# Optimization experiments

Measured on AMD Instinct MI355X. Metric: run time of the kernel, lower is better.

Reference implementation:

```python
import jax, jax.numpy as jnp
import numpy as np

B, S, L, Q = 128, 200, 50, 20   # batch, story sentences, sentence len, query len
V, D, K = 50000, 128, 3          # vocab, embed dim, n_hops


def _pe(J, d):
    # position encoding l_kj = (1 - j/J) - (k/d)(1 - 2j/J), 1-indexed
    j = jnp.arange(1, J + 1, dtype=jnp.float32)[:, None]
    k = jnp.arange(1, d + 1, dtype=jnp.float32)[None, :]
    return 1.0 - j / J - (k / d) * (1.0 - 2.0 * j / J)  # (J, d)


def setup_inputs() -> dict:
    key = jax.random.key(0)
    ks = jax.random.split(key, 5)
    story = jax.random.randint(ks[0], (B, S, L), 0, V)
    query = jax.random.randint(ks[1], (B, Q), 0, V)
    # K+1 embedding tables (adjacent weight sharing: A^{k+1} = C^k), sigma=0.1, padding row 0 zeroed
    embs = (jax.random.normal(ks[2], (K + 1, V, D)) * 0.1).at[:, 0, :].set(0.0)
    TA = jax.random.normal(ks[3], (K, S, D)) * 0.1
    TC = jax.random.normal(ks[4], (K, S, D)) * 0.1
    return {"story": story, "query": query, "embs": embs, "TA": TA, "TC": TC}


def reference(story, query, embs, TA, TC):
    d = embs.shape[-1]
    pe_s = _pe(story.shape[-1], d)   # (L, D)
    pe_q = _pe(query.shape[-1], d)   # (Q, D)
    n_hops = TA.shape[0]

    # query embedding with PE: (B, Q, D) * (Q, D) -> sum over Q -> (B, D)
    u = (jnp.take(embs[0], query, axis=0) * pe_q).sum(axis=1)

    for hop in range(n_hops):
        # gather + PE multiply + sum over words + temporal encoding: (B, S, D)
        m = (jnp.take(embs[hop], story, axis=0) * pe_s).sum(axis=2) + TA[hop]
        c = (jnp.take(embs[hop + 1], story, axis=0) * pe_s).sum(axis=2) + TC[hop]
        # attention over memory slots
        p = jax.nn.softmax(jnp.einsum('bsd,bd->bs', m, u), axis=-1)  # (B, S)
        o = jnp.einsum('bs,bsd->bd', p, c)                            # (B, D)
        u = u + o

    # final projection W = embeddings[n_hops].weight -> logits (B, V)
    return u @ embs[n_hops].T
```

## Files before the change

kernel.cpp:

```cpp
#include <hip/hip_runtime.h>

#define B 128
#define S 200
#define LW 50
#define Q 20
#define V 50000
#define D 128
#define NH 3
#define VD (V * D)
#define BSD (B * S * D)
#define BS (B * S)

typedef __bf16 bf16x8 __attribute__((ext_vector_type(8)));
typedef float f32x4 __attribute__((ext_vector_type(4)));
typedef unsigned int u32x4 __attribute__((ext_vector_type(4)));

__device__ __forceinline__ unsigned int f2bf_rne(float f) {
  union { float f; unsigned int u; } c; c.f = f;
  return (c.u + 0x7FFFu + ((c.u >> 16) & 1u)) >> 16;
}
__device__ __forceinline__ unsigned int pack2(float a, float b) {
  return f2bf_rne(a) | (f2bf_rne(b) << 16);
}
__device__ __forceinline__ float bf_lo(unsigned int q) {
  union { unsigned int u; float f; } c; c.u = q << 16; return c.f;
}
__device__ __forceinline__ float bf_hi(unsigned int q) {
  union { unsigned int u; float f; } c; c.u = q & 0xFFFF0000u; return c.f;
}

__global__ __launch_bounds__(256) void k_repack(
    const float* __restrict__ embs, unsigned int* __restrict__ ESM) {
  int v = blockIdx.x * 4 + (threadIdx.x >> 6);
  int l = threadIdx.x & 63;
  int s = l >> 4, c = l & 15;
#pragma unroll
  for (int k = 0; k < 4; ++k) {
    const float2 e = *(const float2*)(embs + (size_t)k * VD + (size_t)v * D + 2 * l);
    ESM[((size_t)(k * 4 + s) * V + v) * 16 + c] = pack2(e.x, e.y);
  }
}

__global__ __launch_bounds__(256) void k_story16(
    const int* __restrict__ story, unsigned short* __restrict__ story16) {
  int i = blockIdx.x * 256 + threadIdx.x;
  int4 v = ((const int4*)story)[i];
  ushort4 o;
  o.x = (unsigned short)v.x; o.y = (unsigned short)v.y;
  o.z = (unsigned short)v.z; o.w = (unsigned short)v.w;
  ((ushort4*)story16)[i] = o;
}

__global__ __launch_bounds__(256) void k_packT(
    const float* __restrict__ TA, const float* __restrict__ TC,
    unsigned int* __restrict__ TAp, unsigned int* __restrict__ TCp) {
  int idx = blockIdx.x * 256 + threadIdx.x;
  int row = idx >> 6;
  int u = idx & 63;
  int d0 = 32 * (u >> 4) + 2 * (u & 15);
  const float2 a = *(const float2*)(TA + (size_t)row * D + d0);
  const float2 c = *(const float2*)(TC + (size_t)row * D + d0);
  TAp[idx] = pack2(a.x, a.y);
  TCp[idx] = pack2(c.x, c.y);
}

__global__ __launch_bounds__(256) void k_gather_slice(
    const unsigned short* __restrict__ story16,
    const u32x4* __restrict__ ESM4, unsigned int* __restrict__ Gp, int phase) {
  __shared__ __align__(16) unsigned short sidx[4][800];
  int unit = blockIdx.x & 7;
  int k = 2 * phase + (unit >> 2);
  int s = unit & 3;
  int widx = blockIdx.x >> 3;
  int w = threadIdx.x >> 6;
  int l = threadIdx.x & 63;
  int g = l >> 2;
  int q = l & 3;
  const u32x4* src4 = ESM4 + (size_t)(k * 4 + s) * V * 4;
  int d0 = s * 32 + 8 * q;

  int sent16 = widx * 64 + w * 16;
  const u32x4* st4 = (const u32x4*)(story16 + sent16 * LW);
  u32x4* dst4 = (u32x4*)sidx[w];
#pragma unroll
  for (int m = 0; m < 2; ++m) {
    int e = l + m * 64;
    if (e < 100) dst4[e] = __builtin_nontemporal_load(st4 + e);
  }
  const unsigned int* wrow32 = (const unsigned int*)(sidx[w] + g * LW);
  float SA[8] = {0.f, 0.f, 0.f, 0.f, 0.f, 0.f, 0.f, 0.f};
  float SB[8] = {0.f, 0.f, 0.f, 0.f, 0.f, 0.f, 0.f, 0.f};
#pragma unroll
  for (int jb = 0; jb < 5; ++jb) {
    unsigned int ip[5];
#pragma unroll
    for (int i = 0; i < 5; ++i) ip[i] = wrow32[jb * 5 + i];
    u32x4 qv[10];
#pragma unroll
    for (int i = 0; i < 5; ++i) {
      qv[2 * i + 0] = src4[(size_t)(ip[i] & 0xFFFFu) * 4 + q];
      qv[2 * i + 1] = src4[(size_t)(ip[i] >> 16) * 4 + q];
    }
#pragma unroll
    for (int i = 0; i < 10; ++i) {
      int j = jb * 10 + i;
      float jj = (float)(j + 1) * (1.0f / LW);
      float al = 1.0f - jj;
      float bl = 2.0f * jj - 1.0f;
      u32x4 v = qv[i];
      float ee[8];
      ee[0] = bf_lo(v.x); ee[1] = bf_hi(v.x);
      ee[2] = bf_lo(v.y); ee[3] = bf_hi(v.y);
      ee[4] = bf_lo(v.z); ee[5] = bf_hi(v.z);
      ee[6] = bf_lo(v.w); ee[7] = bf_hi(v.w);
#pragma unroll
      for (int ii = 0; ii < 8; ++ii) {
        SA[ii] += ee[ii] * al;
        SB[ii] += ee[ii] * bl;
      }
    }
  }
  float kd[8];
#pragma unroll
  for (int i = 0; i < 8; ++i) kd[i] = (float)(d0 + i + 1) * (1.0f / D);
  int sent = sent16 + g;
  u32x4 og;
  og.x = pack2(SA[0] + kd[0] * SB[0], SA[1] + kd[1] * SB[1]);
  og.y = pack2(SA[2] + kd[2] * SB[2], SA[3] + kd[3] * SB[3]);
  og.z = pack2(SA[4] + kd[4] * SB[4], SA[5] + kd[5] * SB[5]);
  og.w = pack2(SA[6] + kd[6] * SB[6], SA[7] + kd[7] * SB[7]);
  __builtin_nontemporal_store(
      og, (u32x4*)(Gp + ((size_t)k * BS + sent) * 64 + s * 16) + q);
}

__global__ __launch_bounds__(1024) void k_hops(
    const unsigned int* __restrict__ G, const unsigned int* __restrict__ TAp,
    const unsigned int* __restrict__ TCp, const int* __restrict__ query,
    const float* __restrict__ emb0, unsigned int* __restrict__ ubf) {
  __shared__ float su[D];
  __shared__ float sp[S];
  __shared__ float sred[2];
  __shared__ float4 oacc[32][32];
  int b = blockIdx.x;
  int t = threadIdx.x;
  if (t < D) {
    float kd = (float)(t + 1) * (1.0f / D);
    float acc = 0.f;
    for (int q = 0; q < Q; ++q) {
      int idx = query[b * Q + q];
      float jj = (float)(q + 1) * (1.0f / Q);
      float pe = 1.0f - jj - kd * (1.0f - 2.0f * jj);
      acc += emb0[(size_t)idx * D + t] * pe;
    }
    su[t] = acc;
  }
  __syncthreads();
  for (int hop = 0; hop < NH; ++hop) {
    const unsigned int* Gm = G + ((size_t)hop * BS + (size_t)b * S) * 64;
    const unsigned int* Gc = G + ((size_t)(hop + 1) * BS + (size_t)b * S) * 64;
    const unsigned int* ta = TAp + (size_t)hop * S * 64;
    const unsigned int* tc = TCp + (size_t)hop * S * 64;
    if (t < 4 * S) {
      int sl = t >> 2, p = t & 3;
      const uint2* gr = (const uint2*)(Gm + (size_t)sl * 64 + p * 16);
      const uint2* tr = (const uint2*)(ta + (size_t)sl * 64 + p * 16);
      float sc = 0.f;
#pragma unroll
      for (int i = 0; i < 8; ++i) {
        uint2 g2 = gr[i];
        uint2 t2 = tr[i];
        int dd = p * 32 + 4 * i;
        sc += (bf_lo(g2.x) + bf_lo(t2.x)) * su[dd + 0];
        sc += (bf_hi(g2.x) + bf_hi(t2.x)) * su[dd + 1];
        sc += (bf_lo(g2.y) + bf_lo(t2.y)) * su[dd + 2];
        sc += (bf_hi(g2.y) + bf_hi(t2.y)) * su[dd + 3];
      }
      sc += __shfl_xor(sc, 1);
      sc += __shfl_xor(sc, 2);
      if (p == 0) sp[sl] = sc;
    }
    __syncthreads();
    if (t < 64) {
      float mx = -1e30f;
      for (int s = t; s < S; s += 64) mx = fmaxf(mx, sp[s]);
#pragma unroll
      for (int off = 1; off < 64; off <<= 1) mx = fmaxf(mx, __shfl_xor(mx, off));
      float sum = 0.f;
      for (int s = t; s < S; s += 64) sum += expf(sp[s] - mx);
#pragma unroll
      for (int off = 1; off < 64; off <<= 1) sum += __shfl_xor(sum, off);
      if (t == 0) { sred[0] = mx; sred[1] = sum; }
    }
    __syncthreads();
    float mx = sred[0];
    float inv = 1.0f / sred[1];
    if (t < S) sp[t] = expf(sp[t] - mx) * inv;
    __syncthreads();
    {
      int g = t >> 5, c = t & 31;
      float4 o4 = {0.f, 0.f, 0.f, 0.f};
      for (int s = g; s < S; s += 32) {
        float p = sp[s];
        uint2 g2 = *(const uint2*)(Gc + (size_t)s * 64 + 2 * c);
        uint2 t2 = *(const uint2*)(tc + (size_t)s * 64 + 2 * c);
        o4.x += p * (bf_lo(g2.x) + bf_lo(t2.x));
        o4.y += p * (bf_hi(g2.x) + bf_hi(t2.x));
        o4.z += p * (bf_lo(g2.y) + bf_lo(t2.y));
        o4.w += p * (bf_hi(g2.y) + bf_hi(t2.y));
      }
      oacc[g][c] = o4;
    }
    __syncthreads();
    if (t < 32) {
      int d0 = (t >> 3) * 32 + (t & 7) * 4;
      float4 o = oacc[0][t];
#pragma unroll
      for (int g = 1; g < 32; ++g) {
        float4 x = oacc[g][t];
        o.x += x.x; o.y += x.y; o.z += x.z; o.w += x.w;
      }
      su[d0 + 0] += o.x;
      su[d0 + 1] += o.y;
      su[d0 + 2] += o.z;
      su[d0 + 3] += o.w;
    }
    __syncthreads();
  }
  if (t < 64) ubf[b * 64 + t] = pack2(su[2 * t], su[2 * t + 1]);
}

__global__ __launch_bounds__(256) void k_logits_mfma(
    const uint4* __restrict__ ubf,
    const uint4* __restrict__ esm,
    float* __restrict__ out) {
  int wid = threadIdx.x >> 6;
  int l = threadIdx.x & 63;
  int lr = l & 15;
  int lk = l >> 4;
  int vbase = blockIdx.x * 128 + wid * 32;
  uint4 bfrag[2][4];
#pragma unroll
  for (int vs = 0; vs < 2; ++vs) {
    int v = vbase + vs * 16 + lr;
    if (v >= V) v = V - 1;
#pragma unroll
    for (int kk = 0; kk < 4; ++kk)
      bfrag[vs][kk] = esm[((size_t)(12 + kk) * V + v) * 4 + lk];
  }
  f32x4 acc[2][8];
#pragma unroll
  for (int vs = 0; vs < 2; ++vs)
#pragma unroll
    for (int m = 0; m < 8; ++m) {
      f32x4 z = {0.f, 0.f, 0.f, 0.f};
      acc[vs][m] = z;
    }
#pragma unroll
  for (int m = 0; m < 8; ++m) {
    uint4 afrag[4];
#pragma unroll
    for (int kk = 0; kk < 4; ++kk)
      afrag[kk] = ubf[(m * 16 + lr) * 16 + kk * 4 + lk];
#pragma unroll
    for (int vs = 0; vs < 2; ++vs)
#pragma unroll
      for (int kk = 0; kk < 4; ++kk)
        acc[vs][m] = __builtin_amdgcn_mfma_f32_16x16x32_bf16(
            __builtin_bit_cast(bf16x8, afrag[kk]),
            __builtin_bit_cast(bf16x8, bfrag[vs][kk]), acc[vs][m], 0, 0, 0);
  }
#pragma unroll
  for (int vs = 0; vs < 2; ++vs) {
    int v = vbase + vs * 16 + lr;
    if (v < V) {
#pragma unroll
      for (int m = 0; m < 8; ++m)
#pragma unroll
        for (int r = 0; r < 4; ++r)
          out[(size_t)(m * 16 + lk * 4 + r) * V + v] = acc[vs][m][r];
    }
  }
}

__global__ __launch_bounds__(128) void k_gather_query(
    const int* __restrict__ query, const float* __restrict__ embs,
    float* __restrict__ u) {
  int b = blockIdx.x;
  int d = threadIdx.x;
  float kd = (float)(d + 1) / (float)D;
  float acc = 0.f;
  for (int q = 0; q < Q; ++q) {
    int idx = query[b * Q + q];
    float jj = (float)(q + 1) / (float)Q;
    float pe = 1.0f - jj - kd * (1.0f - 2.0f * jj);
    acc += embs[(size_t)idx * D + d] * pe;
  }
  u[b * D + d] = acc;
}

__global__ __launch_bounds__(128) void k_gather_story(
    const int* __restrict__ story, const float* __restrict__ embs,
    float* __restrict__ G) {
  int bs = blockIdx.x;
  int d = threadIdx.x;
  const int* w = story + bs * LW;
  float kd = (float)(d + 1) / (float)D;
  float a0 = 0.f, a1 = 0.f, a2 = 0.f, a3 = 0.f;
  for (int l = 0; l < LW; ++l) {
    int idx = w[l];
    float jj = (float)(l + 1) / (float)LW;
    float pe = 1.0f - jj - kd * (1.0f - 2.0f * jj);
    size_t base = (size_t)idx * D + d;
    a0 += embs[base] * pe;
    a1 += embs[base + (size_t)VD] * pe;
    a2 += embs[base + (size_t)(2 * VD)] * pe;
    a3 += embs[base + (size_t)(3 * VD)] * pe;
  }
  size_t o = (size_t)bs * D + d;
  G[o] = a0;
  G[o + (size_t)BSD] = a1;
  G[o + (size_t)(2 * BSD)] = a2;
  G[o + (size_t)(3 * BSD)] = a3;
}

__global__ __launch_bounds__(256) void k_hops_f32(
    const float* __restrict__ G, const float* __restrict__ TA,
    const float* __restrict__ TC, float* __restrict__ u) {
  __shared__ float su[D];
  __shared__ float sp[S];
  __shared__ float sred[2];
  int b = blockIdx.x;
  int t = threadIdx.x;
  if (t < D) su[t] = u[b * D + t];
  __syncthreads();
  for (int hop = 0; hop < NH; ++hop) {
    const float* Gm = G + (size_t)hop * BSD + (size_t)b * S * D;
    const float* Gc = G + (size_t)(hop + 1) * BSD + (size_t)b * S * D;
    const float* ta = TA + hop * S * D;
    const float* tc = TC + hop * S * D;
    if (t < S) {
      float sc = 0.f;
      for (int d = 0; d < D; ++d) sc += (Gm[t * D + d] + ta[t * D + d]) * su[d];
      sp[t] = sc;
    }
    __syncthreads();
    if (t < 64) {
      float mx = -1e30f;
      for (int s = t; s < S; s += 64) mx = fmaxf(mx, sp[s]);
#pragma unroll
      for (int off = 1; off < 64; off <<= 1) mx = fmaxf(mx, __shfl_xor(mx, off));
      float sum = 0.f;
      for (int s = t; s < S; s += 64) sum += expf(sp[s] - mx);
#pragma unroll
      for (int off = 1; off < 64; off <<= 1) sum += __shfl_xor(sum, off);
      if (t == 0) { sred[0] = mx; sred[1] = sum; }
    }
    __syncthreads();
    float mx = sred[0];
    float inv = 1.0f / sred[1];
    if (t < S) sp[t] = expf(sp[t] - mx) * inv;
    __syncthreads();
    if (t < D) {
      float o = 0.f;
      for (int s = 0; s < S; ++s) o += sp[s] * (Gc[s * D + t] + tc[s * D + t]);
      su[t] += o;
    }
    __syncthreads();
  }
  if (t < D) u[b * D + t] = su[t];
}

__global__ __launch_bounds__(256) void k_logits_f32(
    const float* __restrict__ u, const float* __restrict__ e3,
    float* __restrict__ out) {
  __shared__ float sE[64][129];
  __shared__ float sU[64][129];
  int v0 = blockIdx.x * 64;
  int b0 = blockIdx.y * 64;
  int t = threadIdx.x;
  for (int i = 0; i < 32; ++i) {
    int lin = i * 256 + t;
    int r = lin >> 7, c = lin & 127;
    int v = v0 + r;
    sE[r][c] = (v < V) ? e3[(size_t)v * D + c] : 0.f;
    sU[r][c] = u[(b0 + r) * D + c];
  }
  __syncthreads();
  int tv = (t & 15) * 4;
  int tb = (t >> 4) * 4;
  float acc[4][4] = {};
  for (int d = 0; d < D; ++d) {
    float ev[4], ub[4];
#pragma unroll
    for (int i = 0; i < 4; ++i) ev[i] = sE[tv + i][d];
#pragma unroll
    for (int j = 0; j < 4; ++j) ub[j] = sU[tb + j][d];
#pragma unroll
    for (int j = 0; j < 4; ++j)
#pragma unroll
      for (int i = 0; i < 4; ++i) acc[j][i] += ub[j] * ev[i];
  }
  for (int j = 0; j < 4; ++j)
    for (int i = 0; i < 4; ++i) {
      int v = v0 + tv + i;
      if (v < V) out[(size_t)(b0 + tb + j) * V + v] = acc[j][i];
    }
}

extern "C" void kernel_launch(void* const* d_in, const int* in_sizes, int n_in,
                              void* d_out, int out_size, void* d_ws,
                              size_t ws_size, hipStream_t stream) {
  (void)in_sizes; (void)n_in; (void)out_size;
  const int* story = (const int*)d_in[0];
  const int* query = (const int*)d_in[1];
  const float* embs = (const float*)d_in[2];
  const float* TA = (const float*)d_in[3];
  const float* TC = (const float*)d_in[4];
  float* out = (float*)d_out;

  const size_t esm_bytes = (size_t)16 * V * 16 * 4;
  const size_t g_bytes = (size_t)4 * BS * 64 * 4;
  const size_t ub_bytes = (size_t)B * 64 * 4;
  const size_t s16_bytes = (size_t)BS * LW * 2;
  const size_t tp_bytes = (size_t)NH * S * 64 * 4;

  if (ws_size >= esm_bytes + g_bytes + ub_bytes + s16_bytes + 2 * tp_bytes) {
    char* p = (char*)d_ws;
    unsigned int* ESM = (unsigned int*)p;      p += esm_bytes;
    unsigned int* Gp = (unsigned int*)p;       p += g_bytes;
    unsigned int* ubf = (unsigned int*)p;      p += ub_bytes;
    unsigned short* story16 = (unsigned short*)p;  p += s16_bytes;
    unsigned int* TAp = (unsigned int*)p;      p += tp_bytes;
    unsigned int* TCp = (unsigned int*)p;

    k_repack<<<V / 4, 256, 0, stream>>>(embs, ESM);
    k_story16<<<BS * LW / 4 / 256, 256, 0, stream>>>(story, story16);
    k_packT<<<NH * S * 64 / 256, 256, 0, stream>>>(TA, TC, TAp, TCp);
    k_gather_slice<<<3200, 256, 0, stream>>>(story16, (const u32x4*)ESM, Gp, 0);
    k_gather_slice<<<3200, 256, 0, stream>>>(story16, (const u32x4*)ESM, Gp, 1);
    k_hops<<<B, 1024, 0, stream>>>(Gp, TAp, TCp, query, embs, ubf);
    k_logits_mfma<<<(V + 127) / 128, 256, 0, stream>>>(
        (const uint4*)ubf, (const uint4*)ESM, out);
  } else {
    float* G = (float*)d_ws;
    float* u = G + 4 * (size_t)BSD;
    k_gather_query<<<B, D, 0, stream>>>(query, embs, u);
    k_gather_story<<<B * S, D, 0, stream>>>(story, embs, G);
    k_hops_f32<<<B, 256, 0, stream>>>(G, TA, TC, u);
    k_logits_f32<<<dim3((V + 63) / 64, B / 64), 256, 0, stream>>>(
        u, embs + 3 * (size_t)VD, out);
  }
}
```

Baseline: 174.2 us.

## Overlap embedding repack of tables 2-3 with first gather phase; split logits over batch

The single repack kernel is split in two. Tables 0-1 are repacked first, and the repack of tables 2-3 is fused into the phase-0 gather launch as extra blocks, so that bandwidth-bound conversion overlaps with the latency-bound gather. The repack path now uses nontemporal loads and stores. The logits MFMA kernel gets a second grid dimension that splits the 128 batch rows into two halves, which halves accumulator registers and doubles parallelism but reloads the B fragments twice.

```diff
diff --git a/kernel.cpp b/kernel.cpp
--- a/kernel.cpp
+++ b/kernel.cpp
@@ -13,6 +13,7 @@
 
 typedef __bf16 bf16x8 __attribute__((ext_vector_type(8)));
 typedef float f32x4 __attribute__((ext_vector_type(4)));
+typedef float f32x2 __attribute__((ext_vector_type(2)));
 typedef unsigned int u32x4 __attribute__((ext_vector_type(4)));
 
 __device__ __forceinline__ unsigned int f2bf_rne(float f) {
@@ -29,13 +30,14 @@
   union { unsigned int u; float f; } c; c.u = q & 0xFFFF0000u; return c.f;
 }
 
-__global__ __launch_bounds__(256) void k_repack(
-    const float* __restrict__ embs, unsigned int* __restrict__ ESM) {
+__global__ __launch_bounds__(256) void k_repack_pair(
+    const float* __restrict__ embs, unsigned int* __restrict__ ESM, int kbase) {
   int v = blockIdx.x * 4 + (threadIdx.x >> 6);
   int l = threadIdx.x & 63;
   int s = l >> 4, c = l & 15;
 #pragma unroll
-  for (int k = 0; k < 4; ++k) {
+  for (int kk = 0; kk < 2; ++kk) {
+    int k = kbase + kk;
     const float2 e = *(const float2*)(embs + (size_t)k * VD + (size_t)v * D + 2 * l);
     ESM[((size_t)(k * 4 + s) * V + v) * 16 + c] = pack2(e.x, e.y);
   }
@@ -64,30 +66,24 @@
   TCp[idx] = pack2(c.x, c.y);
 }
 
-__global__ __launch_bounds__(256) void k_gather_slice(
+__device__ __forceinline__ void gather_body(
+    unsigned short* sidx_w,
     const unsigned short* __restrict__ story16,
-    const u32x4* __restrict__ ESM4, unsigned int* __restrict__ Gp, int phase) {
-  __shared__ __align__(16) unsigned short sidx[4][800];
-  int unit = blockIdx.x & 7;
-  int k = 2 * phase + (unit >> 2);
-  int s = unit & 3;
-  int widx = blockIdx.x >> 3;
-  int w = threadIdx.x >> 6;
-  int l = threadIdx.x & 63;
+    const u32x4* __restrict__ ESM4, unsigned int* __restrict__ Gp,
+    int k, int s, int widx, int w, int l) {
   int g = l >> 2;
   int q = l & 3;
   const u32x4* src4 = ESM4 + (size_t)(k * 4 + s) * V * 4;
   int d0 = s * 32 + 8 * q;
-
   int sent16 = widx * 64 + w * 16;
   const u32x4* st4 = (const u32x4*)(story16 + sent16 * LW);
-  u32x4* dst4 = (u32x4*)sidx[w];
+  u32x4* dst4 = (u32x4*)sidx_w;
 #pragma unroll
   for (int m = 0; m < 2; ++m) {
     int e = l + m * 64;
     if (e < 100) dst4[e] = __builtin_nontemporal_load(st4 + e);
   }
-  const unsigned int* wrow32 = (const unsigned int*)(sidx[w] + g * LW);
+  const unsigned int* wrow32 = (const unsigned int*)(sidx_w + g * LW);
   float SA[8] = {0.f, 0.f, 0.f, 0.f, 0.f, 0.f, 0.f, 0.f};
   float SB[8] = {0.f, 0.f, 0.f, 0.f, 0.f, 0.f, 0.f, 0.f};
 #pragma unroll
@@ -131,6 +127,48 @@
   og.w = pack2(SA[6] + kd[6] * SB[6], SA[7] + kd[7] * SB[7]);
   __builtin_nontemporal_store(
       og, (u32x4*)(Gp + ((size_t)k * BS + sent) * 64 + s * 16) + q);
+}
+
+__global__ __launch_bounds__(256) void k_gather_slice(
+    const unsigned short* __restrict__ story16,
+    const u32x4* __restrict__ ESM4, unsigned int* __restrict__ Gp, int phase) {
+  __shared__ __align__(16) unsigned short sidx[4][800];
+  int unit = blockIdx.x & 7;
+  int k = 2 * phase + (unit >> 2);
+  int s = unit & 3;
+  int widx = blockIdx.x >> 3;
+  int w = threadIdx.x >> 6;
+  int l = threadIdx.x & 63;
+  gather_body(sidx[w], story16, ESM4, Gp, k, s, widx, w, l);
+}
+
+__global__ __launch_bounds__(256) void k_gather_fused0(
+    const unsigned short* __restrict__ story16,
+    const u32x4* __restrict__ ESM4, unsigned int* __restrict__ Gp,
+    const float* __restrict__ embs, unsigned int* __restrict__ ESM) {
+  __shared__ __align__(16) unsigned short sidx[4][800];
+  int bi = blockIdx.x;
+  if (bi < 3200) {
+    int unit = bi & 7;
+    int k = unit >> 2;
+    int s = unit & 3;
+    int widx = bi >> 3;
+    int w = threadIdx.x >> 6;
+    int l = threadIdx.x & 63;
+    gather_body(sidx[w], story16, ESM4, Gp, k, s, widx, w, l);
+  } else {
+    int r = bi - 3200;
+    int v = r * 4 + (threadIdx.x >> 6);
+    int l = threadIdx.x & 63;
+    int s = l >> 4, c = l & 15;
+#pragma unroll
+    for (int k = 2; k < 4; ++k) {
+      f32x2 e = __builtin_nontemporal_load(
+          (const f32x2*)(embs + (size_t)k * VD + (size_t)v * D + 2 * l));
+      __builtin_nontemporal_store(
+          pack2(e.x, e.y), ESM + ((size_t)(k * 4 + s) * V + v) * 16 + c);
+    }
+  }
 }
 
 __global__ __launch_bounds__(1024) void k_hops(
@@ -238,6 +276,7 @@
   int lr = l & 15;
   int lk = l >> 4;
   int vbase = blockIdx.x * 128 + wid * 32;
+  int mbase = blockIdx.y * 4;
   uint4 bfrag[2][4];
 #pragma unroll
   for (int vs = 0; vs < 2; ++vs) {
@@ -247,20 +286,21 @@
     for (int kk = 0; kk < 4; ++kk)
       bfrag[vs][kk] = esm[((size_t)(12 + kk) * V + v) * 4 + lk];
   }
-  f32x4 acc[2][8];
+  f32x4 acc[2][4];
 #pragma unroll
   for (int vs = 0; vs < 2; ++vs)
 #pragma unroll
-    for (int m = 0; m < 8; ++m) {
+    for (int m = 0; m < 4; ++m) {
       f32x4 z = {0.f, 0.f, 0.f, 0.f};
       acc[vs][m] = z;
     }
 #pragma unroll
-  for (int m = 0; m < 8; ++m) {
+  for (int m = 0; m < 4; ++m) {
+    int gm = mbase + m;
     uint4 afrag[4];
 #pragma unroll
     for (int kk = 0; kk < 4; ++kk)
-      afrag[kk] = ubf[(m * 16 + lr) * 16 + kk * 4 + lk];
+      afrag[kk] = ubf[(gm * 16 + lr) * 16 + kk * 4 + lk];
 #pragma unroll
     for (int vs = 0; vs < 2; ++vs)
 #pragma unroll
@@ -274,10 +314,10 @@
     int v = vbase + vs * 16 + lr;
     if (v < V) {
 #pragma unroll
-      for (int m = 0; m < 8; ++m)
+      for (int m = 0; m < 4; ++m)
 #pragma unroll
         for (int r = 0; r < 4; ++r)
-          out[(size_t)(m * 16 + lk * 4 + r) * V + v] = acc[vs][m][r];
+          out[(size_t)((mbase + m) * 16 + lk * 4 + r) * V + v] = acc[vs][m][r];
     }
   }
 }
@@ -433,13 +473,14 @@
     unsigned int* TAp = (unsigned int*)p;      p += tp_bytes;
     unsigned int* TCp = (unsigned int*)p;
 
-    k_repack<<<V / 4, 256, 0, stream>>>(embs, ESM);
     k_story16<<<BS * LW / 4 / 256, 256, 0, stream>>>(story, story16);
     k_packT<<<NH * S * 64 / 256, 256, 0, stream>>>(TA, TC, TAp, TCp);
-    k_gather_slice<<<3200, 256, 0, stream>>>(story16, (const u32x4*)ESM, Gp, 0);
+    k_repack_pair<<<V / 4, 256, 0, stream>>>(embs, ESM, 0);
+    k_gather_fused0<<<3200 + V / 4, 256, 0, stream>>>(
+        story16, (const u32x4*)ESM, Gp, embs, ESM);
     k_gather_slice<<<3200, 256, 0, stream>>>(story16, (const u32x4*)ESM, Gp, 1);
     k_hops<<<B, 1024, 0, stream>>>(Gp, TAp, TCp, query, embs, ubf);
-    k_logits_mfma<<<(V + 127) / 128, 256, 0, stream>>>(
+    k_logits_mfma<<<dim3((V + 127) / 128, 2), 256, 0, stream>>>(
         (const uint4*)ubf, (const uint4*)ESM, out);
   } else {
     float* G = (float*)d_ws;
```

After: 187.5 us. 1.08x slower.
